# Kernel tuning notes

Hardware: AMD Instinct MI355X
Metric: run time of the kernel (lower is better)

Reference implementation:

```python
import jax, jax.numpy as jnp
import numpy as np

B, T, V, E, H, DE = 64, 52, 10000, 512, 512, 2048


def _lstm_cell(x, h, c, w_ih, w_hh, b_ih, b_hh):
    # torch.nn.LSTMCell gate order: i, f, g, o
    gates = x @ w_ih.T + h @ w_hh.T + b_ih + b_hh
    i, f, g, o = jnp.split(gates, 4, axis=-1)
    c2 = jax.nn.sigmoid(f) * c + jax.nn.sigmoid(i) * jnp.tanh(g)
    h2 = jax.nn.sigmoid(o) * jnp.tanh(c2)
    return h2, c2


def _run_dir(emb_seq, img, lens, p1, p2, fc_w, fc_b):
    # emb_seq: [B, Td, E]; img: [B, H]; lens: [B] sorted descending.
    # The torch loop slices h[:batch_size_t]; since lens is sorted descending,
    # that is equivalent to masking updates where t >= (len-1). Rows that fall
    # out of the active prefix are never read again, and their predictions stay 0.
    Bd, Td = emb_seq.shape[0], emb_seq.shape[1]
    Hd = img.shape[1]
    mask = jnp.arange(Td)[None, :] < (lens - 1)[:, None]  # [B, Td]
    z = jnp.zeros((Bd, Hd), emb_seq.dtype)

    def step(carry, xs):
        h, c, h1, c1 = carry
        x, m = xs
        m2 = m[:, None]
        hn, cn = _lstm_cell(x, h, c, *p1)
        h1n, c1n = _lstm_cell(jnp.concatenate([hn, img], axis=1), h1, c1, *p2)
        carry = (jnp.where(m2, hn, h), jnp.where(m2, cn, c),
                 jnp.where(m2, h1n, h1), jnp.where(m2, c1n, c1))
        preds = jnp.where(m2, h1n @ fc_w.T + fc_b, 0.0)  # [B, V]
        return carry, preds

    _, preds = jax.lax.scan(step, (z, z, z, z), (emb_seq.transpose(1, 0, 2), mask.T))
    return preds.transpose(1, 0, 2)  # [B, Td, V]


def setup_inputs():
    key = jax.random.key(0)
    ks = iter(jax.random.split(key, 48))

    def u(shape, a=-0.1, b=0.1):
        return jax.random.uniform(next(ks), shape, minval=a, maxval=b, dtype=jnp.float32)

    inp = {}
    inp['encoder_out'] = jax.random.normal(next(ks), (B, DE), dtype=jnp.float32)
    inp['encoded_captions'] = jax.random.randint(next(ks), (B, T), 0, V)
    cl = jax.random.randint(next(ks), (B, 1), 2, T + 1)
    inp['caption_lengths'] = cl.at[0, 0].set(T)  # ensure max decode length = T-1
    # embeddings (uniform -0.1..0.1 per init_weights)
    inp['emb_w'] = u((V, E))
    inp['emb_r_w'] = u((V, E))
    # LSTM cells: torch default init uniform(-1/sqrt(H), 1/sqrt(H))
    kH = 1.0 / np.sqrt(H)
    for name, din in [('1', E), ('2', 2 * H), ('r1', E), ('r2', 2 * H)]:
        inp['w_ih' + name] = u((4 * H, din), -kH, kH)
        inp['w_hh' + name] = u((4 * H, H), -kH, kH)
        inp['b_ih' + name] = u((4 * H,), -kH, kH)
        inp['b_hh' + name] = u((4 * H,), -kH, kH)
    kD = 1.0 / np.sqrt(DE)
    inp['img_f_w'] = u((H, DE), -kD, kD)
    inp['img_f_b'] = u((H,), -kD, kD)
    inp['img_b_w'] = u((H, DE), -kD, kD)
    inp['img_b_b'] = u((H,), -kD, kD)
    inp['fc_w'] = u((V, H))
    inp['fc_b'] = jnp.zeros((V,), jnp.float32)
    inp['fcr_w'] = u((V, H))
    inp['fcr_b'] = jnp.zeros((V,), jnp.float32)
    return inp


def reference(encoder_out, encoded_captions, caption_lengths, emb_w, emb_r_w,
              w_ih1, w_hh1, b_ih1, b_hh1, w_ih2, w_hh2, b_ih2, b_hh2,
              w_ihr1, w_hhr1, b_ihr1, b_hhr1, w_ihr2, w_hhr2, b_ihr2, b_hhr2,
              img_f_w, img_f_b, img_b_w, img_b_b, fc_w, fc_b, fcr_w, fcr_b):
    lens = caption_lengths[:, 0]
    order = jnp.argsort(-lens)  # descending, stable (jax argsort is stable)
    lens = lens[order]
    enc = encoder_out[order]
    caps = encoded_captions[order]
    Tc = caps.shape[1]
    # per-row reversal of the first len tokens; rest zero (matches torch loop)
    j = jnp.arange(Tc)[None, :]
    valid = j < lens[:, None]
    rev_idx = jnp.where(valid, lens[:, None] - 1 - j, 0)
    caps_rev = jnp.where(valid, jnp.take_along_axis(caps, rev_idx, axis=1), 0)
    emb = emb_w[caps]          # [B, T, E]
    emb_r = emb_r_w[caps_rev]  # [B, T, E]
    img_f = enc @ img_f_w.T + img_f_b
    img_r = enc @ img_b_w.T + img_b_b
    Td = Tc - 1  # max(decode_lengths); setup guarantees max(lens) == T
    preds = _run_dir(emb[:, :Td], img_f, lens,
                     (w_ih1, w_hh1, b_ih1, b_hh1), (w_ih2, w_hh2, b_ih2, b_hh2), fc_w, fc_b)
    preds_r = _run_dir(emb_r[:, :Td], img_r, lens,
                       (w_ihr1, w_hhr1, b_ihr1, b_hhr1), (w_ihr2, w_hhr2, b_ihr2, b_hhr2), fcr_w, fcr_b)
    return preds, preds_r, caps, caps_rev, lens - 1, order
```

## Files before the change

kernel.cpp:

```cpp
#include <hip/hip_runtime.h>
#include <stdint.h>

#define B64   64
#define T52   52
#define TD    51
#define V10K  10000
#define MP    3328
#define MR    3264
#define NPFC  10112

typedef float  f32x4  __attribute__((ext_vector_type(4)));
typedef __bf16 bf16x8 __attribute__((ext_vector_type(8)));
typedef unsigned int u32x4 __attribute__((ext_vector_type(4)));
typedef unsigned short ushort_t;

__device__ inline unsigned short f2bf(float f) {
  unsigned u = __builtin_bit_cast(unsigned, f);
  u += 0x7fffu + ((u >> 16) & 1u);
  return (unsigned short)(u >> 16);
}
__device__ inline unsigned pack2(float a, float b) {
  return (unsigned)f2bf(a) | ((unsigned)f2bf(b) << 16);
}
__device__ inline float sigm(float x) { return 1.f / (1.f + expf(-x)); }

__device__ inline void store2_sc(ushort_t* p, unsigned v) {
  asm volatile("global_store_short %0, %1, off sc1" :: "v"(p), "v"(v) : "memory");
}
__device__ inline void loadA16(const ushort_t* a, u32x4 (&h)[16]) {
  asm volatile(
    "global_load_dwordx4 %0,  %16, off sc1\n\t"
    "global_load_dwordx4 %1,  %16, off offset:64 sc1\n\t"
    "global_load_dwordx4 %2,  %16, off offset:128 sc1\n\t"
    "global_load_dwordx4 %3,  %16, off offset:192 sc1\n\t"
    "global_load_dwordx4 %4,  %16, off offset:256 sc1\n\t"
    "global_load_dwordx4 %5,  %16, off offset:320 sc1\n\t"
    "global_load_dwordx4 %6,  %16, off offset:384 sc1\n\t"
    "global_load_dwordx4 %7,  %16, off offset:448 sc1\n\t"
    "global_load_dwordx4 %8,  %16, off offset:512 sc1\n\t"
    "global_load_dwordx4 %9,  %16, off offset:576 sc1\n\t"
    "global_load_dwordx4 %10, %16, off offset:640 sc1\n\t"
    "global_load_dwordx4 %11, %16, off offset:704 sc1\n\t"
    "global_load_dwordx4 %12, %16, off offset:768 sc1\n\t"
    "global_load_dwordx4 %13, %16, off offset:832 sc1\n\t"
    "global_load_dwordx4 %14, %16, off offset:896 sc1\n\t"
    "global_load_dwordx4 %15, %16, off offset:960 sc1\n\t"
    "s_waitcnt vmcnt(0)"
    : "=&v"(h[0]),"=&v"(h[1]),"=&v"(h[2]),"=&v"(h[3]),
      "=&v"(h[4]),"=&v"(h[5]),"=&v"(h[6]),"=&v"(h[7]),
      "=&v"(h[8]),"=&v"(h[9]),"=&v"(h[10]),"=&v"(h[11]),
      "=&v"(h[12]),"=&v"(h[13]),"=&v"(h[14]),"=&v"(h[15])
    : "v"(a) : "memory");
}
__device__ inline void loadA32(const ushort_t* a, const ushort_t* b,
                               u32x4 (&ha)[16], u32x4 (&hb)[16]) {
  asm volatile(
    "global_load_dwordx4 %0,  %32, off sc1\n\t"
    "global_load_dwordx4 %1,  %32, off offset:64 sc1\n\t"
    "global_load_dwordx4 %2,  %32, off offset:128 sc1\n\t"
    "global_load_dwordx4 %3,  %32, off offset:192 sc1\n\t"
    "global_load_dwordx4 %4,  %32, off offset:256 sc1\n\t"
    "global_load_dwordx4 %5,  %32, off offset:320 sc1\n\t"
    "global_load_dwordx4 %6,  %32, off offset:384 sc1\n\t"
    "global_load_dwordx4 %7,  %32, off offset:448 sc1\n\t"
    "global_load_dwordx4 %8,  %32, off offset:512 sc1\n\t"
    "global_load_dwordx4 %9,  %32, off offset:576 sc1\n\t"
    "global_load_dwordx4 %10, %32, off offset:640 sc1\n\t"
    "global_load_dwordx4 %11, %32, off offset:704 sc1\n\t"
    "global_load_dwordx4 %12, %32, off offset:768 sc1\n\t"
    "global_load_dwordx4 %13, %32, off offset:832 sc1\n\t"
    "global_load_dwordx4 %14, %32, off offset:896 sc1\n\t"
    "global_load_dwordx4 %15, %32, off offset:960 sc1\n\t"
    "global_load_dwordx4 %16, %33, off sc1\n\t"
    "global_load_dwordx4 %17, %33, off offset:64 sc1\n\t"
    "global_load_dwordx4 %18, %33, off offset:128 sc1\n\t"
    "global_load_dwordx4 %19, %33, off offset:192 sc1\n\t"
    "global_load_dwordx4 %20, %33, off offset:256 sc1\n\t"
    "global_load_dwordx4 %21, %33, off offset:320 sc1\n\t"
    "global_load_dwordx4 %22, %33, off offset:384 sc1\n\t"
    "global_load_dwordx4 %23, %33, off offset:448 sc1\n\t"
    "global_load_dwordx4 %24, %33, off offset:512 sc1\n\t"
    "global_load_dwordx4 %25, %33, off offset:576 sc1\n\t"
    "global_load_dwordx4 %26, %33, off offset:640 sc1\n\t"
    "global_load_dwordx4 %27, %33, off offset:704 sc1\n\t"
    "global_load_dwordx4 %28, %33, off offset:768 sc1\n\t"
    "global_load_dwordx4 %29, %33, off offset:832 sc1\n\t"
    "global_load_dwordx4 %30, %33, off offset:896 sc1\n\t"
    "global_load_dwordx4 %31, %33, off offset:960 sc1\n\t"
    "s_waitcnt vmcnt(0)"
    : "=&v"(ha[0]),"=&v"(ha[1]),"=&v"(ha[2]),"=&v"(ha[3]),
      "=&v"(ha[4]),"=&v"(ha[5]),"=&v"(ha[6]),"=&v"(ha[7]),
      "=&v"(ha[8]),"=&v"(ha[9]),"=&v"(ha[10]),"=&v"(ha[11]),
      "=&v"(ha[12]),"=&v"(ha[13]),"=&v"(ha[14]),"=&v"(ha[15]),
      "=&v"(hb[0]),"=&v"(hb[1]),"=&v"(hb[2]),"=&v"(hb[3]),
      "=&v"(hb[4]),"=&v"(hb[5]),"=&v"(hb[6]),"=&v"(hb[7]),
      "=&v"(hb[8]),"=&v"(hb[9]),"=&v"(hb[10]),"=&v"(hb[11]),
      "=&v"(hb[12]),"=&v"(hb[13]),"=&v"(hb[14]),"=&v"(hb[15])
    : "v"(a), "v"(b) : "memory");
}

__global__ void k_prep(const int* __restrict__ cl, const int* __restrict__ caps,
                       float* __restrict__ out_caps, float* __restrict__ out_capr,
                       float* __restrict__ out_lm1, float* __restrict__ out_ord,
                       int* __restrict__ order_i, int* __restrict__ lensm1_i,
                       int* __restrict__ nvtab, int* __restrict__ capsS,
                       int* __restrict__ capsRev, int* __restrict__ cumtab,
                       int* __restrict__ rowmap)
{
  __shared__ int L[64], O[64], Ls_s[64], Cum[65];
  __shared__ int C_s[64][T52];
  int i = threadIdx.x;
  L[i] = cl[i];
  __syncthreads();
  if (i == 0) {
    for (int a = 0; a < 64; ++a) O[a] = a;
    for (int a = 1; a < 64; ++a) {
      int key = O[a], kl = L[key], b = a - 1;
      while (b >= 0 && L[O[b]] < kl) { O[b + 1] = O[b]; --b; }
      O[b + 1] = key;
    }
  }
  __syncthreads();
  int src = O[i];
  int Ls  = L[src];
  Ls_s[i] = Ls;
  order_i[i]  = src;
  lensm1_i[i] = Ls - 1;
  out_lm1[i]  = (float)(Ls - 1);
  out_ord[i]  = (float)src;
  for (int t = 0; t < T52; ++t) {
    int c = caps[src * T52 + t];
    C_s[i][t] = c;
    capsS[i * T52 + t]    = c;
    out_caps[i * T52 + t] = (float)c;
  }
  __syncthreads();
  for (int j = 0; j < T52; ++j) {
    int rv = (j < Ls) ? C_s[i][Ls - 1 - j] : 0;
    capsRev[i * T52 + j]  = rv;
    out_capr[i * T52 + j] = (float)rv;
  }
  if (i == 0) {
    int s = 0;
    for (int b = 0; b < 64; ++b) { Cum[b] = s; s += Ls_s[b] - 1; }
    Cum[64] = s;
  }
  __syncthreads();
  cumtab[i] = Cum[i];
  if (i == 0) cumtab[64] = Cum[64];
  for (int t = 0; t < Ls - 1; ++t) rowmap[Cum[i] + t] = i * TD + t;
  if (i < TD) {
    int nv = 0;
    for (int r = 0; r < 64; ++r) nv += (Ls_s[r] - 1 > i) ? 1 : 0;
    nvtab[i] = nv;
  }
}

__global__ void k_convert(const float* __restrict__ w_ih1, const float* __restrict__ w_ihr1,
                          const float* __restrict__ fc_w, const float* __restrict__ fcr_w,
                          const float* __restrict__ b_ih1, const float* __restrict__ b_hh1,
                          const float* __restrict__ b_ihr1, const float* __restrict__ b_hhr1,
                          const float* __restrict__ w_hh1, const float* __restrict__ w_hhr1,
                          const float* __restrict__ w_ih2, const float* __restrict__ w_ihr2,
                          const float* __restrict__ w_hh2, const float* __restrict__ w_hhr2,
                          const float* __restrict__ img_f_w, const float* __restrict__ img_b_w,
                          const float* __restrict__ b_ih2, const float* __restrict__ b_hh2,
                          const float* __restrict__ b_ihr2, const float* __restrict__ b_hhr2,
                          const float* __restrict__ enc, const int* __restrict__ order_i,
                          ushort_t* __restrict__ wih1bf, ushort_t* __restrict__ fcwbf,
                          ushort_t* __restrict__ whh1bf, ushort_t* __restrict__ wih2Lbf,
                          ushort_t* __restrict__ whh2bf, ushort_t* __restrict__ wih2Ibf,
                          ushort_t* __restrict__ imgwbf, ushort_t* __restrict__ encbf,
                          float* __restrict__ biasg1, float* __restrict__ biasg2)
{
  long long gid = (long long)blockIdx.x * blockDim.x + threadIdx.x;
  const long long C1 = 2048LL * 512 / 8;
  const long long CF = (long long)NPFC * 512 / 8;
  const long long bs  = 2 * C1 + 2 * CF;
  const long long bs2 = bs + 6 * C1;
  const long long bs3 = bs2 + 2 * C1;
  const long long bs4 = bs3 + 2 * C1;
  const long long bs5 = bs4 + 32768;
  if (gid < 2 * C1) {
    int dir = gid >= C1; long long cid = gid - (long long)dir * C1;
    const float* s = (dir ? w_ihr1 : w_ih1) + cid * 8;
    ushort_t* d = wih1bf + (long long)dir * 2048 * 512 + cid * 8;
    uint4 v;
    v.x = pack2(s[0], s[1]); v.y = pack2(s[2], s[3]);
    v.z = pack2(s[4], s[5]); v.w = pack2(s[6], s[7]);
    *(uint4*)d = v;
  } else if (gid < bs) {
    long long g2 = gid - 2 * C1; int dir = g2 >= CF;
    long long cid = g2 - (long long)dir * CF;
    long long row = cid >> 6; int k8 = (int)(cid & 63) * 8;
    ushort_t* d = fcwbf + (long long)dir * NPFC * 512 + row * 512 + k8;
    uint4 v;
    if (row < V10K) {
      const float* s = (dir ? fcr_w : fc_w) + row * 512 + k8;
      v.x = pack2(s[0], s[1]); v.y = pack2(s[2], s[3]);
      v.z = pack2(s[4], s[5]); v.w = pack2(s[6], s[7]);
    } else { v.x = v.y = v.z = v.w = 0u; }
    *(uint4*)d = v;
  } else if (gid < bs2) {
    long long e = gid - bs;
    int arr = (int)(e / (2 * C1));
    long long d2 = e - (long long)arr * 2 * C1;
    int dir = d2 >= C1;
    long long cid = d2 - (long long)dir * C1;
    long long row = cid >> 6; int k8 = (int)(cid & 63) * 8;
    const float* s;
    ushort_t* d;
    if (arr == 0)      { s = (dir ? w_hhr1 : w_hh1) + row * 512  + k8; d = whh1bf; }
    else if (arr == 1) { s = (dir ? w_ihr2 : w_ih2) + row * 1024 + k8; d = wih2Lbf; }
    else               { s = (dir ? w_hhr2 : w_hh2) + row * 512  + k8; d = whh2bf; }
    d += (long long)dir * 2048 * 512 + cid * 8;
    uint4 v;
    v.x = pack2(s[0], s[1]); v.y = pack2(s[2], s[3]);
    v.z = pack2(s[4], s[5]); v.w = pack2(s[6], s[7]);
    *(uint4*)d = v;
  } else if (gid < bs3) {
    long long e = gid - bs2; int dir = e >= C1;
    long long cid = e - (long long)dir * C1;
    long long row = cid >> 6; int k8 = (int)(cid & 63) * 8;
    const float* s = (dir ? w_ihr2 : w_ih2) + row * 1024 + 512 + k8;
    ushort_t* d = wih2Ibf + (long long)dir * 2048 * 512 + cid * 8;
    uint4 v;
    v.x = pack2(s[0], s[1]); v.y = pack2(s[2], s[3]);
    v.z = pack2(s[4], s[5]); v.w = pack2(s[6], s[7]);
    *(uint4*)d = v;
  } else if (gid < bs4) {
    long long e = gid - bs3; int dir = e >= C1;
    long long cid = e - (long long)dir * C1;
    long long row = cid >> 8; int c8 = (int)(cid & 255) * 8;
    const float* s = (dir ? img_b_w : img_f_w) + row * 2048 + c8;
    ushort_t* d = imgwbf + (long long)dir * 512 * 2048 + cid * 8;
    uint4 v;
    v.x = pack2(s[0], s[1]); v.y = pack2(s[2], s[3]);
    v.z = pack2(s[4], s[5]); v.w = pack2(s[6], s[7]);
    *(uint4*)d = v;
  } else if (gid < bs5) {
    long long cid = gid - bs4;
    int m = (int)(cid >> 8); int c8 = (int)(cid & 255) * 8;
    const float* s = enc + (long long)order_i[m & 63] * 2048 + c8;
    ushort_t* d = encbf + cid * 8;
    uint4 v;
    v.x = pack2(s[0], s[1]); v.y = pack2(s[2], s[3]);
    v.z = pack2(s[4], s[5]); v.w = pack2(s[6], s[7]);
    *(uint4*)d = v;
  } else {
    long long g3 = gid - bs5;
    if (g3 < 4096) {
      int dir = g3 >= 2048; int j = (int)(g3 & 2047);
      biasg1[dir * 2048 + j] = dir ? (b_ihr1[j] + b_hhr1[j]) : (b_ih1[j] + b_hh1[j]);
    } else if (g3 < 8192) {
      long long g4 = g3 - 4096;
      int dir = g4 >= 2048; int j = (int)(g4 & 2047);
      biasg2[dir * 2048 + j] = dir ? (b_ihr2[j] + b_hhr2[j]) : (b_ih2[j] + b_hh2[j]);
    }
  }
}

__global__ void k_gather(const float* __restrict__ emb_w, const float* __restrict__ emb_r_w,
                         const int* __restrict__ capsS, const int* __restrict__ capsRev,
                         const int* __restrict__ rowmap, const int* __restrict__ cumtab,
                         ushort_t* __restrict__ embA)
{
  long long gid = (long long)blockIdx.x * 256 + threadIdx.x;
  const long long CPD = (long long)MP * 512 / 8;
  if (gid >= 2 * CPD) return;
  int dir = gid >= CPD; long long cid = gid - (long long)dir * CPD;
  int c = (int)(cid >> 6); int k8 = (int)(cid & 63) * 8;
  ushort_t* d = embA + (long long)dir * MP * 512 + (long long)c * 512 + k8;
  uint4 v;
  if (c < cumtab[64]) {
    int m = rowmap[c];
    int b = m / TD, t = m - b * TD;
    int row = dir ? capsRev[b * T52 + t] : capsS[b * T52 + t];
    const float* s = (dir ? emb_r_w : emb_w) + (long long)row * 512 + k8;
    v.x = pack2(s[0], s[1]); v.y = pack2(s[2], s[3]);
    v.z = pack2(s[4], s[5]); v.w = pack2(s[6], s[7]);
  } else { v.x = v.y = v.z = v.w = 0u; }
  *(uint4*)d = v;
}

template<int MODE>
__global__ __launch_bounds__(256)
void k_gemm(const ushort_t* __restrict__ A0, long long As,
            const ushort_t* __restrict__ B0, long long Bs,
            const float* __restrict__ bias0, const float* __restrict__ bias1,
            void* __restrict__ out0, long long Os,
            int Nreal, int K, const int* __restrict__ mlim)
{
  long long tm = (long long)blockIdx.x * 128;
  if (mlim && tm >= mlim[64]) return;
  __shared__ ushort_t Ab[128 * 32];
  __shared__ ushort_t Bb[128 * 32];
  int dirz = blockIdx.z;
  const ushort_t* A = A0 + dirz * As;
  const ushort_t* Bm = B0 + dirz * Bs;
  const float* bias = dirz ? bias1 : bias0;
  int tid = threadIdx.x;
  int lane = tid & 63, wid = tid >> 6;
  int wr = wid >> 1, wc = wid & 1;
  long long tn = (long long)blockIdx.y * 128;
  f32x4 acc[4][4] = {};
  int c0 = tid, c1 = tid + 256;
  const ushort_t* Ag0 = A + (tm + (c0 >> 2)) * K + (c0 & 3) * 8;
  const ushort_t* Ag1 = A + (tm + (c1 >> 2)) * K + (c1 & 3) * 8;
  const ushort_t* Bg0 = Bm + (tn + (c0 >> 2)) * K + (c0 & 3) * 8;
  const ushort_t* Bg1 = Bm + (tn + (c1 >> 2)) * K + (c1 & 3) * 8;
  int KK = K >> 5;
  for (int kk = 0; kk < KK; ++kk) {
    uint4 va0 = *(const uint4*)(Ag0 + kk * 32);
    uint4 va1 = *(const uint4*)(Ag1 + kk * 32);
    uint4 vb0 = *(const uint4*)(Bg0 + kk * 32);
    uint4 vb1 = *(const uint4*)(Bg1 + kk * 32);
    __syncthreads();
    *(uint4*)&Ab[c0 * 8] = va0;
    *(uint4*)&Ab[c1 * 8] = va1;
    *(uint4*)&Bb[c0 * 8] = vb0;
    *(uint4*)&Bb[c1 * 8] = vb1;
    __syncthreads();
    int koff = (lane >> 4) * 8;
    bf16x8 av[4], bv[4];
    #pragma unroll
    for (int mi = 0; mi < 4; ++mi)
      av[mi] = *(const bf16x8*)&Ab[(wr * 64 + mi * 16 + (lane & 15)) * 32 + koff];
    #pragma unroll
    for (int ni = 0; ni < 4; ++ni)
      bv[ni] = *(const bf16x8*)&Bb[(wc * 64 + ni * 16 + (lane & 15)) * 32 + koff];
    #pragma unroll
    for (int mi = 0; mi < 4; ++mi)
      #pragma unroll
      for (int ni = 0; ni < 4; ++ni)
        acc[mi][ni] = __builtin_amdgcn_mfma_f32_16x16x32_bf16(av[mi], bv[ni], acc[mi][ni], 0, 0, 0);
  }
  #pragma unroll
  for (int mi = 0; mi < 4; ++mi) {
    #pragma unroll
    for (int rr = 0; rr < 4; ++rr) {
      long long m = tm + wr * 64 + mi * 16 + ((lane >> 4) * 4) + rr;
      if (MODE == 0) {
        float* orow = (float*)out0 + dirz * Os + m * (long long)Nreal;
        #pragma unroll
        for (int ni = 0; ni < 4; ++ni) {
          int n = (int)tn + wc * 64 + ni * 16 + (lane & 15);
          orow[n] = acc[mi][ni][rr] + bias[n];
        }
      } else if (MODE == 2) {
        float bm = bias[m];
        float* orow = (float*)out0 + dirz * Os + m * (long long)Nreal;
        #pragma unroll
        for (int ni = 0; ni < 4; ++ni) {
          int n = (int)tn + wc * 64 + ni * 16 + (lane & 15);
          if (n < Nreal) orow[n] = acc[mi][ni][rr] + bm;
        }
      } else {
        ushort_t* orow = (ushort_t*)out0 + dirz * Os + m * (long long)Nreal;
        #pragma unroll
        for (int ni = 0; ni < 4; ++ni) {
          int n = (int)tn + wc * 64 + ni * 16 + (lane & 15);
          orow[n] = f2bf(acc[mi][ni][rr] + bias[n]);
        }
      }
    }
  }
}

__global__ __launch_bounds__(256)
void k_fc(const ushort_t* __restrict__ A0, const ushort_t* __restrict__ B0,
          const float* __restrict__ bias0, const float* __restrict__ bias1,
          float* __restrict__ out0, const int* __restrict__ rowmap,
          const int* __restrict__ cumtab)
{
  const long long PRED = (long long)MR * V10K;
  int Mc = cumtab[64];
  long long tm = (long long)blockIdx.x * 128;
  if (tm >= Mc) return;
  __shared__ ushort_t Ab[128 * 32];
  __shared__ ushort_t Bb[128 * 32];
  int dirz = blockIdx.z;
  const ushort_t* A = A0 + (long long)dirz * MP * 512;
  const ushort_t* Bm = B0 + (long long)dirz * NPFC * 512;
  const float* bias = dirz ? bias1 : bias0;
  float* out = out0 + (long long)dirz * PRED;
  int tid = threadIdx.x;
  int lane = tid & 63, wid = tid >> 6;
  int wr = wid >> 1, wc = wid & 1;
  long long tn = (long long)blockIdx.y * 128;
  f32x4 acc[4][4] = {};
  int c0 = tid, c1 = tid + 256;
  const ushort_t* Ag0 = A + (tm + (c0 >> 2)) * 512 + (c0 & 3) * 8;
  const ushort_t* Ag1 = A + (tm + (c1 >> 2)) * 512 + (c1 & 3) * 8;
  const ushort_t* Bg0 = Bm + (tn + (c0 >> 2)) * 512 + (c0 & 3) * 8;
  const ushort_t* Bg1 = Bm + (tn + (c1 >> 2)) * 512 + (c1 & 3) * 8;
  for (int kk = 0; kk < 16; ++kk) {
    uint4 va0 = *(const uint4*)(Ag0 + kk * 32);
    uint4 va1 = *(const uint4*)(Ag1 + kk * 32);
    uint4 vb0 = *(const uint4*)(Bg0 + kk * 32);
    uint4 vb1 = *(const uint4*)(Bg1 + kk * 32);
    __syncthreads();
    *(uint4*)&Ab[c0 * 8] = va0;
    *(uint4*)&Ab[c1 * 8] = va1;
    *(uint4*)&Bb[c0 * 8] = vb0;
    *(uint4*)&Bb[c1 * 8] = vb1;
    __syncthreads();
    int koff = (lane >> 4) * 8;
    bf16x8 av[4], bv[4];
    #pragma unroll
    for (int mi = 0; mi < 4; ++mi)
      av[mi] = *(const bf16x8*)&Ab[(wr * 64 + mi * 16 + (lane & 15)) * 32 + koff];
    #pragma unroll
    for (int ni = 0; ni < 4; ++ni)
      bv[ni] = *(const bf16x8*)&Bb[(wc * 64 + ni * 16 + (lane & 15)) * 32 + koff];
    #pragma unroll
    for (int mi = 0; mi < 4; ++mi)
      #pragma unroll
      for (int ni = 0; ni < 4; ++ni)
        acc[mi][ni] = __builtin_amdgcn_mfma_f32_16x16x32_bf16(av[mi], bv[ni], acc[mi][ni], 0, 0, 0);
  }
  #pragma unroll
  for (int mi = 0; mi < 4; ++mi) {
    #pragma unroll
    for (int rr = 0; rr < 4; ++rr) {
      long long c = tm + wr * 64 + mi * 16 + ((lane >> 4) * 4) + rr;
      if (c < Mc) {
        int m = rowmap[c];
        float* orow = out + (long long)m * V10K;
        #pragma unroll
        for (int ni = 0; ni < 4; ++ni) {
          int n = (int)tn + wc * 64 + ni * 16 + (lane & 15);
          if (n < V10K) orow[n] = acc[mi][ni][rr] + bias[n];
        }
      }
    }
  }
}

__global__ __launch_bounds__(256)
void k_zero(float* __restrict__ outF, const int* __restrict__ lensm1_i)
{
  const long long PRED = (long long)MR * V10K;
  int m = blockIdx.x;
  int b = m / TD, t = m - b * TD;
  if (t < lensm1_i[b]) return;
  float4 z = {0.f, 0.f, 0.f, 0.f};
  float* r0 = outF + (long long)m * V10K;
  float* r1 = outF + PRED + (long long)m * V10K;
  for (int i = threadIdx.x; i < 2500; i += 256) {
    ((float4*)r0)[i] = z;
    ((float4*)r1)[i] = z;
  }
}

__global__ __launch_bounds__(128, 1)
void k_rec(const ushort_t* __restrict__ whh1bf, const ushort_t* __restrict__ wih2Lbf,
           const ushort_t* __restrict__ whh2bf, const float* __restrict__ xg1,
           const float* __restrict__ xg2imgT,
           ushort_t* __restrict__ h1hist,
           ushort_t* __restrict__ h2buf,
           ushort_t* __restrict__ h2allbf,
           const int* __restrict__ nvtab, const int* __restrict__ cumtab,
           int* __restrict__ slots)
{
  const int bid = blockIdx.x;
  const bool isL2 = bid >= 128;
  const int idx = isL2 ? bid - 128 : bid;
  const int dir = idx >> 6, sub = idx & 63, half = sub >> 5, ht = sub & 31;
  const int tid = threadIdx.x;
  const int lane = tid & 63, mt = tid >> 6;
  const int l15 = lane & 15, l4 = lane >> 4;
  const int jl = ht * 16 + l15;
  const int rbase = half * 32 + mt * 16;
  const int r0 = rbase + l4 * 4;

  __shared__ ushort_t Wl[32768];
  __shared__ ushort_t Wi[32768];
  __shared__ int nv_s[64];
  __shared__ int cum_s[64];

  {
    const ushort_t* src = (isL2 ? whh2bf : whh1bf) + (long long)dir * 2048 * 512;
    #pragma unroll
    for (int i = 0; i < 32; ++i) {
      int c = tid + i * 128;
      int nl = c >> 6;
      int kb = (c & 63) * 16;
      int row = (nl >> 4) * 512 + ht * 16 + (nl & 15);
      u32x4 v = *(const u32x4*)(src + (long long)row * 512 + (long long)(c & 63) * 8);
      *(u32x4*)((char*)Wl + nl * 1024 + (kb ^ ((nl & 7) << 4))) = v;
    }
    if (isL2) {
      const ushort_t* src2 = wih2Lbf + (long long)dir * 2048 * 512;
      #pragma unroll
      for (int i = 0; i < 32; ++i) {
        int c = tid + i * 128;
        int nl = c >> 6;
        int kb = (c & 63) * 16;
        int row = (nl >> 4) * 512 + ht * 16 + (nl & 15);
        u32x4 v = *(const u32x4*)(src2 + (long long)row * 512 + (long long)(c & 63) * 8);
        *(u32x4*)((char*)Wi + nl * 1024 + (kb ^ ((nl & 7) << 4))) = v;
      }
    }
    if (tid < TD) nv_s[tid] = nvtab[tid];
    if (tid < 64) cum_s[tid] = cumtab[tid];
  }
  __syncthreads();

  int* aS = slots + (dir * 2 + half) * 32;
  int* bS = slots + 128 + (dir * 2 + half) * 32;

  if (!isL2) {
    f32x4 creg = {0.f, 0.f, 0.f, 0.f};
    for (int t = 0; t < TD; ++t) {
      bool act = (rbase < nv_s[t]);
      float xs[4][4];
      if (act) {
        const float* xb = xg1 + (long long)dir * MP * 2048;
        #pragma unroll
        for (int rr = 0; rr < 4; ++rr) {
          const float* xr = xb + (long long)(cum_s[r0 + rr] + t) * 2048;
          #pragma unroll
          for (int g = 0; g < 4; ++g)
            xs[g][rr] = xr[g * 512 + jl];
        }
      }
      if (t > 0) {
        if (mt == 0) {
          for (;;) {
            int v = __hip_atomic_load(&aS[lane & 31], __ATOMIC_RELAXED, __HIP_MEMORY_SCOPE_AGENT);
            if (__all(v >= t)) break;
          }
        }
        __syncthreads();
      }
      if (act) {
        const ushort_t* hsrc = h1hist + ((long long)t * 2 + dir) * (64 * 512);
        u32x4 hv[16];
        loadA16(hsrc + (long long)(rbase + l15) * 512 + l4 * 8, hv);
        f32x4 acc[4] = {};
        #pragma unroll
        for (int kk = 0; kk < 16; ++kk) {
          bf16x8 av = __builtin_bit_cast(bf16x8, hv[kk]);
          int kb = kk * 64 + l4 * 16;
          #pragma unroll
          for (int g = 0; g < 4; ++g) {
            bf16x8 bv = *(const bf16x8*)((const char*)Wl + (g * 16 + l15) * 1024 + (kb ^ ((l15 & 7) << 4)));
            acc[g] = __builtin_amdgcn_mfma_f32_16x16x32_bf16(av, bv, acc[g], 0, 0, 0);
          }
        }
        ushort_t* hdst = h1hist + ((long long)(t + 1) * 2 + dir) * (64 * 512);
        f32x4 cn;
        #pragma unroll
        for (int rr = 0; rr < 4; ++rr) {
          float gi = acc[0][rr] + xs[0][rr];
          float gf = acc[1][rr] + xs[1][rr];
          float gg = acc[2][rr] + xs[2][rr];
          float go = acc[3][rr] + xs[3][rr];
          float c = sigm(gf) * creg[rr] + sigm(gi) * tanhf(gg);
          float h = sigm(go) * tanhf(c);
          cn[rr] = c;
          store2_sc(hdst + (long long)(r0 + rr) * 512 + jl, (unsigned)f2bf(h));
        }
        creg = cn;
      }
      __syncthreads();
      if (tid == 0)
        __hip_atomic_store(&aS[ht], t + 1, __ATOMIC_RELAXED, __HIP_MEMORY_SCOPE_AGENT);
    }
  } else {
    f32x4 xv2[4];
    {
      const float* xg = xg2imgT + (long long)dir * (2048 * 64);
      #pragma unroll
      for (int g = 0; g < 4; ++g)
        xv2[g] = *(const f32x4*)(xg + (long long)(g * 512 + jl) * 64 + r0);
    }
    f32x4 creg = {0.f, 0.f, 0.f, 0.f};
    for (int t = 0; t < TD; ++t) {
      if (mt == 0) {
        for (;;) {
          int va = __hip_atomic_load(&aS[lane & 31], __ATOMIC_RELAXED, __HIP_MEMORY_SCOPE_AGENT);
          int vb = __hip_atomic_load(&bS[lane & 31], __ATOMIC_RELAXED, __HIP_MEMORY_SCOPE_AGENT);
          if (__all((va >= t + 1) & (vb >= t))) break;
        }
      }
      __syncthreads();
      int nv = nv_s[t];
      if (rbase < nv) {
        const ushort_t* h1s = h1hist + ((long long)(t + 1) * 2 + dir) * (64 * 512);
        const ushort_t* h2s = h2buf + ((long long)((t + 1) & 1) * 2 + dir) * (64 * 512);
        u32x4 ha[16], hb[16];
        loadA32(h1s + (long long)(rbase + l15) * 512 + l4 * 8,
                h2s + (long long)(rbase + l15) * 512 + l4 * 8, ha, hb);
        f32x4 acc[4] = {};
        #pragma unroll
        for (int kk = 0; kk < 16; ++kk) {
          bf16x8 av = __builtin_bit_cast(bf16x8, ha[kk]);
          int kb = kk * 64 + l4 * 16;
          #pragma unroll
          for (int g = 0; g < 4; ++g) {
            bf16x8 bv = *(const bf16x8*)((const char*)Wi + (g * 16 + l15) * 1024 + (kb ^ ((l15 & 7) << 4)));
            acc[g] = __builtin_amdgcn_mfma_f32_16x16x32_bf16(av, bv, acc[g], 0, 0, 0);
          }
        }
        #pragma unroll
        for (int kk = 0; kk < 16; ++kk) {
          bf16x8 av = __builtin_bit_cast(bf16x8, hb[kk]);
          int kb = kk * 64 + l4 * 16;
          #pragma unroll
          for (int g = 0; g < 4; ++g) {
            bf16x8 bv = *(const bf16x8*)((const char*)Wl + (g * 16 + l15) * 1024 + (kb ^ ((l15 & 7) << 4)));
            acc[g] = __builtin_amdgcn_mfma_f32_16x16x32_bf16(av, bv, acc[g], 0, 0, 0);
          }
        }
        ushort_t* h2n = h2buf + ((long long)(t & 1) * 2 + dir) * (64 * 512);
        ushort_t* h2a = h2allbf + (long long)dir * MP * 512;
        f32x4 cn;
        #pragma unroll
        for (int rr = 0; rr < 4; ++rr) {
          float gi = acc[0][rr] + xv2[0][rr];
          float gf = acc[1][rr] + xv2[1][rr];
          float gg = acc[2][rr] + xv2[2][rr];
          float go = acc[3][rr] + xv2[3][rr];
          float c = sigm(gf) * creg[rr] + sigm(gi) * tanhf(gg);
          float h = sigm(go) * tanhf(c);
          cn[rr] = c;
          ushort_t hbb = f2bf(h);
          store2_sc(h2n + (long long)(r0 + rr) * 512 + jl, (unsigned)hbb);
          if (r0 + rr < nv)
            h2a[((long long)(cum_s[r0 + rr] + t)) * 512 + jl] = hbb;
        }
        creg = cn;
      }
      __syncthreads();
      if (tid == 0)
        __hip_atomic_store(&bS[ht], t + 1, __ATOMIC_RELAXED, __HIP_MEMORY_SCOPE_AGENT);
    }
  }
}

extern "C" void kernel_launch(void* const* d_in, const int* in_sizes, int n_in,
                              void* d_out, int out_size, void* d_ws, size_t ws_size,
                              hipStream_t stream)
{
  const float* enc     = (const float*)d_in[0];
  const int*   caps    = (const int*)d_in[1];
  const int*   cl      = (const int*)d_in[2];
  const float* emb_w   = (const float*)d_in[3];
  const float* emb_r_w = (const float*)d_in[4];
  const float* w_ih1   = (const float*)d_in[5];
  const float* w_hh1   = (const float*)d_in[6];
  const float* b_ih1   = (const float*)d_in[7];
  const float* b_hh1   = (const float*)d_in[8];
  const float* w_ih2   = (const float*)d_in[9];
  const float* w_hh2   = (const float*)d_in[10];
  const float* b_ih2   = (const float*)d_in[11];
  const float* b_hh2   = (const float*)d_in[12];
  const float* w_ihr1  = (const float*)d_in[13];
  const float* w_hhr1  = (const float*)d_in[14];
  const float* b_ihr1  = (const float*)d_in[15];
  const float* b_hhr1  = (const float*)d_in[16];
  const float* w_ihr2  = (const float*)d_in[17];
  const float* w_hhr2  = (const float*)d_in[18];
  const float* b_ihr2  = (const float*)d_in[19];
  const float* b_hhr2  = (const float*)d_in[20];
  const float* img_f_w = (const float*)d_in[21];
  const float* img_f_b = (const float*)d_in[22];
  const float* img_b_w = (const float*)d_in[23];
  const float* img_b_b = (const float*)d_in[24];
  const float* fc_w    = (const float*)d_in[25];
  const float* fc_b    = (const float*)d_in[26];
  const float* fcr_w   = (const float*)d_in[27];
  const float* fcr_b   = (const float*)d_in[28];

  float* outF = (float*)d_out;
  const long long PRED = (long long)MR * V10K;
  float* o_caps = outF + 2 * PRED;
  float* o_capr = o_caps + B64 * T52;
  float* o_lm1  = o_capr + B64 * T52;
  float* o_ord  = o_lm1 + B64;
  float*    xg1       = outF;
  ushort_t* whh1bf    = (ushort_t*)(outF + 27500000);
  ushort_t* wih2Lbf   = (ushort_t*)(outF + 28600000);
  ushort_t* whh2bf    = (ushort_t*)(outF + 29700000);
  ushort_t* h1hist    = (ushort_t*)(outF + 31000000);
  ushort_t* wih2Ibf   = (ushort_t*)(outF + 34600000);
  ushort_t* imgwbf    = (ushort_t*)(outF + 35700000);
  ushort_t* encbf     = (ushort_t*)(outF + 36800000);
  ushort_t* imgbf     = (ushort_t*)(outF + 37000000);

  char* w = (char*)d_ws;
  auto alloc = [&](size_t bytes) -> char* {
    char* p = w; w += (bytes + 255) & ~(size_t)255; return p;
  };
  int*      order_i  = (int*)alloc(64 * 4);
  int*      lensm1_i = (int*)alloc(64 * 4);
  int*      nvtab    = (int*)alloc(64 * 4);
  int*      cumtab   = (int*)alloc(65 * 4);
  int*      rowmap   = (int*)alloc(MR * 4);
  int*      capsS    = (int*)alloc(B64 * T52 * 4);
  int*      capsRev  = (int*)alloc(B64 * T52 * 4);
  float*    biasg1   = (float*)alloc(2 * 2048 * 4);
  float*    biasg2   = (float*)alloc(2 * 2048 * 4);
  float*    xg2imgT  = (float*)alloc((size_t)2 * 2048 * 64 * 4);
  char*     stateBase = alloc(262144 + 1024);
  ushort_t* h2buf = (ushort_t*)stateBase;
  int*      slotp = (int*)(stateBase + 262144);
  ushort_t* embA    = (ushort_t*)alloc((size_t)2 * MP * 512 * 2);
  ushort_t* wih1bf  = (ushort_t*)alloc((size_t)2 * 2048 * 512 * 2);
  ushort_t* fcwbf   = (ushort_t*)alloc((size_t)2 * NPFC * 512 * 2);
  ushort_t* h2allbf = (ushort_t*)alloc((size_t)2 * MP * 512 * 2);

  hipMemsetAsync(stateBase, 0, 262144 + 1024, stream);
  hipMemsetAsync(h1hist, 0, 131072, stream);

  k_prep<<<1, 64, 0, stream>>>(cl, caps, o_caps, o_capr, o_lm1, o_ord,
                               order_i, lensm1_i, nvtab, capsS, capsRev,
                               cumtab, rowmap);
  k_convert<<<11360, 256, 0, stream>>>(w_ih1, w_ihr1, fc_w, fcr_w,
                                       b_ih1, b_hh1, b_ihr1, b_hhr1,
                                       w_hh1, w_hhr1, w_ih2, w_ihr2, w_hh2, w_hhr2,
                                       img_f_w, img_b_w, b_ih2, b_hh2, b_ihr2, b_hhr2,
                                       enc, order_i,
                                       wih1bf, fcwbf, whh1bf, wih2Lbf, whh2bf,
                                       wih2Ibf, imgwbf, encbf, biasg1, biasg2);
  k_gather<<<1664, 256, 0, stream>>>(emb_w, emb_r_w, capsS, capsRev,
                                     rowmap, cumtab, embA);
  k_gemm<3><<<dim3(1, 4, 2), 256, 0, stream>>>(encbf, 0LL,
                                               imgwbf, 512LL * 2048,
                                               img_f_b, img_b_b,
                                               imgbf, 128LL * 512,
                                               512, 2048, nullptr);
  k_gemm<2><<<dim3(16, 1, 2), 256, 0, stream>>>(wih2Ibf, 2048LL * 512,
                                                imgbf, 128LL * 512,
                                                biasg2, biasg2 + 2048,
                                                xg2imgT, 2048LL * 64,
                                                64, 512, nullptr);
  k_gemm<0><<<dim3(26, 16, 2), 256, 0, stream>>>(embA, (long long)MP * 512,
                                                 wih1bf, 2048LL * 512,
                                                 biasg1, biasg1 + 2048,
                                                 xg1, (long long)MP * 2048,
                                                 2048, 512, cumtab);
  k_rec<<<256, 128, 0, stream>>>(whh1bf, wih2Lbf, whh2bf, xg1, xg2imgT,
                                 h1hist, h2buf, h2allbf, nvtab, cumtab, slotp);
  k_zero<<<MR, 256, 0, stream>>>(outF, lensm1_i);
  k_fc<<<dim3(26, 79, 2), 256, 0, stream>>>(h2allbf, fcwbf, fc_b, fcr_b,
                                            outF, rowmap, cumtab);
}
```

Measured before the change: 694.0 us.

## Replace block barriers with per-wave flags and split layer-2 waits

```diff
diff --git a/kernel.cpp b/kernel.cpp
--- a/kernel.cpp
+++ b/kernel.cpp
@@ -51,52 +51,6 @@
       "=&v"(h[8]),"=&v"(h[9]),"=&v"(h[10]),"=&v"(h[11]),
       "=&v"(h[12]),"=&v"(h[13]),"=&v"(h[14]),"=&v"(h[15])
     : "v"(a) : "memory");
-}
-__device__ inline void loadA32(const ushort_t* a, const ushort_t* b,
-                               u32x4 (&ha)[16], u32x4 (&hb)[16]) {
-  asm volatile(
-    "global_load_dwordx4 %0,  %32, off sc1\n\t"
-    "global_load_dwordx4 %1,  %32, off offset:64 sc1\n\t"
-    "global_load_dwordx4 %2,  %32, off offset:128 sc1\n\t"
-    "global_load_dwordx4 %3,  %32, off offset:192 sc1\n\t"
-    "global_load_dwordx4 %4,  %32, off offset:256 sc1\n\t"
-    "global_load_dwordx4 %5,  %32, off offset:320 sc1\n\t"
-    "global_load_dwordx4 %6,  %32, off offset:384 sc1\n\t"
-    "global_load_dwordx4 %7,  %32, off offset:448 sc1\n\t"
-    "global_load_dwordx4 %8,  %32, off offset:512 sc1\n\t"
-    "global_load_dwordx4 %9,  %32, off offset:576 sc1\n\t"
-    "global_load_dwordx4 %10, %32, off offset:640 sc1\n\t"
-    "global_load_dwordx4 %11, %32, off offset:704 sc1\n\t"
-    "global_load_dwordx4 %12, %32, off offset:768 sc1\n\t"
-    "global_load_dwordx4 %13, %32, off offset:832 sc1\n\t"
-    "global_load_dwordx4 %14, %32, off offset:896 sc1\n\t"
-    "global_load_dwordx4 %15, %32, off offset:960 sc1\n\t"
-    "global_load_dwordx4 %16, %33, off sc1\n\t"
-    "global_load_dwordx4 %17, %33, off offset:64 sc1\n\t"
-    "global_load_dwordx4 %18, %33, off offset:128 sc1\n\t"
-    "global_load_dwordx4 %19, %33, off offset:192 sc1\n\t"
-    "global_load_dwordx4 %20, %33, off offset:256 sc1\n\t"
-    "global_load_dwordx4 %21, %33, off offset:320 sc1\n\t"
-    "global_load_dwordx4 %22, %33, off offset:384 sc1\n\t"
-    "global_load_dwordx4 %23, %33, off offset:448 sc1\n\t"
-    "global_load_dwordx4 %24, %33, off offset:512 sc1\n\t"
-    "global_load_dwordx4 %25, %33, off offset:576 sc1\n\t"
-    "global_load_dwordx4 %26, %33, off offset:640 sc1\n\t"
-    "global_load_dwordx4 %27, %33, off offset:704 sc1\n\t"
-    "global_load_dwordx4 %28, %33, off offset:768 sc1\n\t"
-    "global_load_dwordx4 %29, %33, off offset:832 sc1\n\t"
-    "global_load_dwordx4 %30, %33, off offset:896 sc1\n\t"
-    "global_load_dwordx4 %31, %33, off offset:960 sc1\n\t"
-    "s_waitcnt vmcnt(0)"
-    : "=&v"(ha[0]),"=&v"(ha[1]),"=&v"(ha[2]),"=&v"(ha[3]),
-      "=&v"(ha[4]),"=&v"(ha[5]),"=&v"(ha[6]),"=&v"(ha[7]),
-      "=&v"(ha[8]),"=&v"(ha[9]),"=&v"(ha[10]),"=&v"(ha[11]),
-      "=&v"(ha[12]),"=&v"(ha[13]),"=&v"(ha[14]),"=&v"(ha[15]),
-      "=&v"(hb[0]),"=&v"(hb[1]),"=&v"(hb[2]),"=&v"(hb[3]),
-      "=&v"(hb[4]),"=&v"(hb[5]),"=&v"(hb[6]),"=&v"(hb[7]),
-      "=&v"(hb[8]),"=&v"(hb[9]),"=&v"(hb[10]),"=&v"(hb[11]),
-      "=&v"(hb[12]),"=&v"(hb[13]),"=&v"(hb[14]),"=&v"(hb[15])
-    : "v"(a), "v"(b) : "memory");
 }
 
 __global__ void k_prep(const int* __restrict__ cl, const int* __restrict__ caps,
@@ -507,8 +461,10 @@
   }
   __syncthreads();
 
-  int* aS = slots + (dir * 2 + half) * 32;
-  int* bS = slots + 128 + (dir * 2 + half) * 32;
+  int* aG = slots + (dir * 2 + half) * 64;
+  int* bG = slots + 256 + (dir * 2 + half) * 64;
+  const int myFlag = (ht << 1) | mt;
+  const int pollIdx = ((lane & 31) << 1) | mt;
 
   if (!isL2) {
     f32x4 creg = {0.f, 0.f, 0.f, 0.f};
@@ -526,13 +482,10 @@
         }
       }
       if (t > 0) {
-        if (mt == 0) {
-          for (;;) {
-            int v = __hip_atomic_load(&aS[lane & 31], __ATOMIC_RELAXED, __HIP_MEMORY_SCOPE_AGENT);
-            if (__all(v >= t)) break;
-          }
-        }
-        __syncthreads();
+        for (;;) {
+          int v = __hip_atomic_load(&aG[pollIdx], __ATOMIC_RELAXED, __HIP_MEMORY_SCOPE_AGENT);
+          if (__all(v >= t)) break;
+        }
       }
       if (act) {
         const ushort_t* hsrc = h1hist + ((long long)t * 2 + dir) * (64 * 512);
@@ -564,9 +517,9 @@
         }
         creg = cn;
       }
-      __syncthreads();
-      if (tid == 0)
-        __hip_atomic_store(&aS[ht], t + 1, __ATOMIC_RELAXED, __HIP_MEMORY_SCOPE_AGENT);
+      asm volatile("s_waitcnt vmcnt(0)" ::: "memory");
+      if (lane == 0)
+        __hip_atomic_store(&aG[myFlag], t + 1, __ATOMIC_RELAXED, __HIP_MEMORY_SCOPE_AGENT);
     }
   } else {
     f32x4 xv2[4];
@@ -578,22 +531,17 @@
     }
     f32x4 creg = {0.f, 0.f, 0.f, 0.f};
     for (int t = 0; t < TD; ++t) {
-      if (mt == 0) {
-        for (;;) {
-          int va = __hip_atomic_load(&aS[lane & 31], __ATOMIC_RELAXED, __HIP_MEMORY_SCOPE_AGENT);
-          int vb = __hip_atomic_load(&bS[lane & 31], __ATOMIC_RELAXED, __HIP_MEMORY_SCOPE_AGENT);
-          if (__all((va >= t + 1) & (vb >= t))) break;
-        }
-      }
-      __syncthreads();
+      bool act = (rbase < nv_s[t]);
       int nv = nv_s[t];
-      if (rbase < nv) {
+      f32x4 acc[4] = {};
+      for (;;) {
+        int v = __hip_atomic_load(&aG[pollIdx], __ATOMIC_RELAXED, __HIP_MEMORY_SCOPE_AGENT);
+        if (__all(v >= t + 1)) break;
+      }
+      if (act) {
         const ushort_t* h1s = h1hist + ((long long)(t + 1) * 2 + dir) * (64 * 512);
-        const ushort_t* h2s = h2buf + ((long long)((t + 1) & 1) * 2 + dir) * (64 * 512);
-        u32x4 ha[16], hb[16];
-        loadA32(h1s + (long long)(rbase + l15) * 512 + l4 * 8,
-                h2s + (long long)(rbase + l15) * 512 + l4 * 8, ha, hb);
-        f32x4 acc[4] = {};
+        u32x4 ha[16];
+        loadA16(h1s + (long long)(rbase + l15) * 512 + l4 * 8, ha);
         #pragma unroll
         for (int kk = 0; kk < 16; ++kk) {
           bf16x8 av = __builtin_bit_cast(bf16x8, ha[kk]);
@@ -604,6 +552,15 @@
             acc[g] = __builtin_amdgcn_mfma_f32_16x16x32_bf16(av, bv, acc[g], 0, 0, 0);
           }
         }
+      }
+      for (;;) {
+        int v = __hip_atomic_load(&bG[pollIdx], __ATOMIC_RELAXED, __HIP_MEMORY_SCOPE_AGENT);
+        if (__all(v >= t)) break;
+      }
+      if (act) {
+        const ushort_t* h2s = h2buf + ((long long)((t + 1) & 1) * 2 + dir) * (64 * 512);
+        u32x4 hb[16];
+        loadA16(h2s + (long long)(rbase + l15) * 512 + l4 * 8, hb);
         #pragma unroll
         for (int kk = 0; kk < 16; ++kk) {
           bf16x8 av = __builtin_bit_cast(bf16x8, hb[kk]);
@@ -633,9 +590,9 @@
         }
         creg = cn;
       }
-      __syncthreads();
-      if (tid == 0)
-        __hip_atomic_store(&bS[ht], t + 1, __ATOMIC_RELAXED, __HIP_MEMORY_SCOPE_AGENT);
+      asm volatile("s_waitcnt vmcnt(0)" ::: "memory");
+      if (lane == 0)
+        __hip_atomic_store(&bG[myFlag], t + 1, __ATOMIC_RELAXED, __HIP_MEMORY_SCOPE_AGENT);
     }
   }
 }
@@ -704,7 +661,7 @@
   float*    biasg1   = (float*)alloc(2 * 2048 * 4);
   float*    biasg2   = (float*)alloc(2 * 2048 * 4);
   float*    xg2imgT  = (float*)alloc((size_t)2 * 2048 * 64 * 4);
-  char*     stateBase = alloc(262144 + 1024);
+  char*     stateBase = alloc(262144 + 4096);
   ushort_t* h2buf = (ushort_t*)stateBase;
   int*      slotp = (int*)(stateBase + 262144);
   ushort_t* embA    = (ushort_t*)alloc((size_t)2 * MP * 512 * 2);
@@ -712,7 +669,7 @@
   ushort_t* fcwbf   = (ushort_t*)alloc((size_t)2 * NPFC * 512 * 2);
   ushort_t* h2allbf = (ushort_t*)alloc((size_t)2 * MP * 512 * 2);
 
-  hipMemsetAsync(stateBase, 0, 262144 + 1024, stream);
+  hipMemsetAsync(stateBase, 0, 262144 + 4096, stream);
   hipMemsetAsync(h1hist, 0, 131072, stream);
 
   k_prep<<<1, 64, 0, stream>>>(cl, caps, o_caps, o_capr, o_lm1, o_ord,
```

New measurement: 724.3 us. +4.4%, slower.

## Fuse embedding gather into convert kernel and widen GEMM K-tile with swizzled LDS

Applied to the files above, without the earlier changes.

```diff
diff --git a/kernel.cpp b/kernel.cpp
--- a/kernel.cpp
+++ b/kernel.cpp
@@ -167,20 +167,26 @@
                           const float* __restrict__ b_ih2, const float* __restrict__ b_hh2,
                           const float* __restrict__ b_ihr2, const float* __restrict__ b_hhr2,
                           const float* __restrict__ enc, const int* __restrict__ order_i,
+                          const float* __restrict__ emb_w, const float* __restrict__ emb_r_w,
+                          const int* __restrict__ capsS, const int* __restrict__ capsRev,
+                          const int* __restrict__ rowmap, const int* __restrict__ cumtab,
                           ushort_t* __restrict__ wih1bf, ushort_t* __restrict__ fcwbf,
                           ushort_t* __restrict__ whh1bf, ushort_t* __restrict__ wih2Lbf,
                           ushort_t* __restrict__ whh2bf, ushort_t* __restrict__ wih2Ibf,
                           ushort_t* __restrict__ imgwbf, ushort_t* __restrict__ encbf,
+                          ushort_t* __restrict__ embA,
                           float* __restrict__ biasg1, float* __restrict__ biasg2)
 {
   long long gid = (long long)blockIdx.x * blockDim.x + threadIdx.x;
   const long long C1 = 2048LL * 512 / 8;
   const long long CF = (long long)NPFC * 512 / 8;
+  const long long CPD = (long long)MP * 512 / 8;
   const long long bs  = 2 * C1 + 2 * CF;
   const long long bs2 = bs + 6 * C1;
   const long long bs3 = bs2 + 2 * C1;
   const long long bs4 = bs3 + 2 * C1;
   const long long bs5 = bs4 + 32768;
+  const long long bs6 = bs5 + 2 * CPD;
   if (gid < 2 * C1) {
     int dir = gid >= C1; long long cid = gid - (long long)dir * C1;
     const float* s = (dir ? w_ihr1 : w_ih1) + cid * 8;
@@ -247,8 +253,23 @@
     v.x = pack2(s[0], s[1]); v.y = pack2(s[2], s[3]);
     v.z = pack2(s[4], s[5]); v.w = pack2(s[6], s[7]);
     *(uint4*)d = v;
+  } else if (gid < bs6) {
+    long long e = gid - bs5;
+    int dir = e >= CPD; long long cid = e - (long long)dir * CPD;
+    int c = (int)(cid >> 6); int k8 = (int)(cid & 63) * 8;
+    ushort_t* d = embA + (long long)dir * MP * 512 + (long long)c * 512 + k8;
+    uint4 v;
+    if (c < cumtab[64]) {
+      int m = rowmap[c];
+      int b = m / TD, t = m - b * TD;
+      int row = dir ? capsRev[b * T52 + t] : capsS[b * T52 + t];
+      const float* s = (dir ? emb_r_w : emb_w) + (long long)row * 512 + k8;
+      v.x = pack2(s[0], s[1]); v.y = pack2(s[2], s[3]);
+      v.z = pack2(s[4], s[5]); v.w = pack2(s[6], s[7]);
+    } else { v.x = v.y = v.z = v.w = 0u; }
+    *(uint4*)d = v;
   } else {
-    long long g3 = gid - bs5;
+    long long g3 = gid - bs6;
     if (g3 < 4096) {
       int dir = g3 >= 2048; int j = (int)(g3 & 2047);
       biasg1[dir * 2048 + j] = dir ? (b_ihr1[j] + b_hhr1[j]) : (b_ih1[j] + b_hh1[j]);
@@ -258,29 +279,6 @@
       biasg2[dir * 2048 + j] = dir ? (b_ihr2[j] + b_hhr2[j]) : (b_ih2[j] + b_hh2[j]);
     }
   }
-}
-
-__global__ void k_gather(const float* __restrict__ emb_w, const float* __restrict__ emb_r_w,
-                         const int* __restrict__ capsS, const int* __restrict__ capsRev,
-                         const int* __restrict__ rowmap, const int* __restrict__ cumtab,
-                         ushort_t* __restrict__ embA)
-{
-  long long gid = (long long)blockIdx.x * 256 + threadIdx.x;
-  const long long CPD = (long long)MP * 512 / 8;
-  if (gid >= 2 * CPD) return;
-  int dir = gid >= CPD; long long cid = gid - (long long)dir * CPD;
-  int c = (int)(cid >> 6); int k8 = (int)(cid & 63) * 8;
-  ushort_t* d = embA + (long long)dir * MP * 512 + (long long)c * 512 + k8;
-  uint4 v;
-  if (c < cumtab[64]) {
-    int m = rowmap[c];
-    int b = m / TD, t = m - b * TD;
-    int row = dir ? capsRev[b * T52 + t] : capsS[b * T52 + t];
-    const float* s = (dir ? emb_r_w : emb_w) + (long long)row * 512 + k8;
-    v.x = pack2(s[0], s[1]); v.y = pack2(s[2], s[3]);
-    v.z = pack2(s[4], s[5]); v.w = pack2(s[6], s[7]);
-  } else { v.x = v.y = v.z = v.w = 0u; }
-  *(uint4*)d = v;
 }
 
 template<int MODE>
@@ -293,8 +291,8 @@
 {
   long long tm = (long long)blockIdx.x * 128;
   if (mlim && tm >= mlim[64]) return;
-  __shared__ ushort_t Ab[128 * 32];
-  __shared__ ushort_t Bb[128 * 32];
+  __shared__ ushort_t Ab[128 * 64];
+  __shared__ ushort_t Bb[128 * 64];
   int dirz = blockIdx.z;
   const ushort_t* A = A0 + dirz * As;
   const ushort_t* Bm = B0 + dirz * Bs;
@@ -304,36 +302,47 @@
   int wr = wid >> 1, wc = wid & 1;
   long long tn = (long long)blockIdx.y * 128;
   f32x4 acc[4][4] = {};
-  int c0 = tid, c1 = tid + 256;
-  const ushort_t* Ag0 = A + (tm + (c0 >> 2)) * K + (c0 & 3) * 8;
-  const ushort_t* Ag1 = A + (tm + (c1 >> 2)) * K + (c1 & 3) * 8;
-  const ushort_t* Bg0 = Bm + (tn + (c0 >> 2)) * K + (c0 & 3) * 8;
-  const ushort_t* Bg1 = Bm + (tn + (c1 >> 2)) * K + (c1 & 3) * 8;
-  int KK = K >> 5;
+  int KK = K >> 6;
   for (int kk = 0; kk < KK; ++kk) {
-    uint4 va0 = *(const uint4*)(Ag0 + kk * 32);
-    uint4 va1 = *(const uint4*)(Ag1 + kk * 32);
-    uint4 vb0 = *(const uint4*)(Bg0 + kk * 32);
-    uint4 vb1 = *(const uint4*)(Bg1 + kk * 32);
+    uint4 va[4], vb[4];
+    #pragma unroll
+    for (int p = 0; p < 4; ++p) {
+      int g = tid + p * 256;
+      int row = g >> 3, gc = g & 7;
+      va[p] = *(const uint4*)(A + (tm + row) * K + kk * 64 + gc * 8);
+      vb[p] = *(const uint4*)(Bm + (tn + row) * K + kk * 64 + gc * 8);
+    }
     __syncthreads();
-    *(uint4*)&Ab[c0 * 8] = va0;
-    *(uint4*)&Ab[c1 * 8] = va1;
-    *(uint4*)&Bb[c0 * 8] = vb0;
-    *(uint4*)&Bb[c1 * 8] = vb1;
+    #pragma unroll
+    for (int p = 0; p < 4; ++p) {
+      int g = tid + p * 256;
+      int row = g >> 3, gc = g & 7;
+      int slot = gc ^ (row & 7);
+      *(uint4*)&Ab[row * 64 + slot * 8] = va[p];
+      *(uint4*)&Bb[row * 64 + slot * 8] = vb[p];
+    }
     __syncthreads();
-    int koff = (lane >> 4) * 8;
-    bf16x8 av[4], bv[4];
-    #pragma unroll
-    for (int mi = 0; mi < 4; ++mi)
-      av[mi] = *(const bf16x8*)&Ab[(wr * 64 + mi * 16 + (lane & 15)) * 32 + koff];
-    #pragma unroll
-    for (int ni = 0; ni < 4; ++ni)
-      bv[ni] = *(const bf16x8*)&Bb[(wc * 64 + ni * 16 + (lane & 15)) * 32 + koff];
-    #pragma unroll
-    for (int mi = 0; mi < 4; ++mi)
+    #pragma unroll
+    for (int sub = 0; sub < 2; ++sub) {
+      bf16x8 av[4], bv[4];
       #pragma unroll
-      for (int ni = 0; ni < 4; ++ni)
-        acc[mi][ni] = __builtin_amdgcn_mfma_f32_16x16x32_bf16(av[mi], bv[ni], acc[mi][ni], 0, 0, 0);
+      for (int mi = 0; mi < 4; ++mi) {
+        int row = wr * 64 + mi * 16 + (lane & 15);
+        int gcol = sub * 4 + (lane >> 4);
+        av[mi] = *(const bf16x8*)&Ab[row * 64 + (gcol ^ (row & 7)) * 8];
+      }
+      #pragma unroll
+      for (int ni = 0; ni < 4; ++ni) {
+        int row = wc * 64 + ni * 16 + (lane & 15);
+        int gcol = sub * 4 + (lane >> 4);
+        bv[ni] = *(const bf16x8*)&Bb[row * 64 + (gcol ^ (row & 7)) * 8];
+      }
+      #pragma unroll
+      for (int mi = 0; mi < 4; ++mi)
+        #pragma unroll
+        for (int ni = 0; ni < 4; ++ni)
+          acc[mi][ni] = __builtin_amdgcn_mfma_f32_16x16x32_bf16(av[mi], bv[ni], acc[mi][ni], 0, 0, 0);
+    }
   }
   #pragma unroll
   for (int mi = 0; mi < 4; ++mi) {
@@ -377,8 +386,8 @@
   int Mc = cumtab[64];
   long long tm = (long long)blockIdx.x * 128;
   if (tm >= Mc) return;
-  __shared__ ushort_t Ab[128 * 32];
-  __shared__ ushort_t Bb[128 * 32];
+  __shared__ ushort_t Ab[128 * 64];
+  __shared__ ushort_t Bb[128 * 64];
   int dirz = blockIdx.z;
   const ushort_t* A = A0 + (long long)dirz * MP * 512;
   const ushort_t* Bm = B0 + (long long)dirz * NPFC * 512;
@@ -389,35 +398,46 @@
   int wr = wid >> 1, wc = wid & 1;
   long long tn = (long long)blockIdx.y * 128;
   f32x4 acc[4][4] = {};
-  int c0 = tid, c1 = tid + 256;
-  const ushort_t* Ag0 = A + (tm + (c0 >> 2)) * 512 + (c0 & 3) * 8;
-  const ushort_t* Ag1 = A + (tm + (c1 >> 2)) * 512 + (c1 & 3) * 8;
-  const ushort_t* Bg0 = Bm + (tn + (c0 >> 2)) * 512 + (c0 & 3) * 8;
-  const ushort_t* Bg1 = Bm + (tn + (c1 >> 2)) * 512 + (c1 & 3) * 8;
-  for (int kk = 0; kk < 16; ++kk) {
-    uint4 va0 = *(const uint4*)(Ag0 + kk * 32);
-    uint4 va1 = *(const uint4*)(Ag1 + kk * 32);
-    uint4 vb0 = *(const uint4*)(Bg0 + kk * 32);
-    uint4 vb1 = *(const uint4*)(Bg1 + kk * 32);
+  for (int kk = 0; kk < 8; ++kk) {
+    uint4 va[4], vb[4];
+    #pragma unroll
+    for (int p = 0; p < 4; ++p) {
+      int g = tid + p * 256;
+      int row = g >> 3, gc = g & 7;
+      va[p] = *(const uint4*)(A + (tm + row) * 512 + kk * 64 + gc * 8);
+      vb[p] = *(const uint4*)(Bm + (tn + row) * 512 + kk * 64 + gc * 8);
+    }
     __syncthreads();
-    *(uint4*)&Ab[c0 * 8] = va0;
-    *(uint4*)&Ab[c1 * 8] = va1;
-    *(uint4*)&Bb[c0 * 8] = vb0;
-    *(uint4*)&Bb[c1 * 8] = vb1;
+    #pragma unroll
+    for (int p = 0; p < 4; ++p) {
+      int g = tid + p * 256;
+      int row = g >> 3, gc = g & 7;
+      int slot = gc ^ (row & 7);
+      *(uint4*)&Ab[row * 64 + slot * 8] = va[p];
+      *(uint4*)&Bb[row * 64 + slot * 8] = vb[p];
+    }
     __syncthreads();
-    int koff = (lane >> 4) * 8;
-    bf16x8 av[4], bv[4];
-    #pragma unroll
-    for (int mi = 0; mi < 4; ++mi)
-      av[mi] = *(const bf16x8*)&Ab[(wr * 64 + mi * 16 + (lane & 15)) * 32 + koff];
-    #pragma unroll
-    for (int ni = 0; ni < 4; ++ni)
-      bv[ni] = *(const bf16x8*)&Bb[(wc * 64 + ni * 16 + (lane & 15)) * 32 + koff];
-    #pragma unroll
-    for (int mi = 0; mi < 4; ++mi)
+    #pragma unroll
+    for (int sub = 0; sub < 2; ++sub) {
+      bf16x8 av[4], bv[4];
       #pragma unroll
-      for (int ni = 0; ni < 4; ++ni)
-        acc[mi][ni] = __builtin_amdgcn_mfma_f32_16x16x32_bf16(av[mi], bv[ni], acc[mi][ni], 0, 0, 0);
+      for (int mi = 0; mi < 4; ++mi) {
+        int row = wr * 64 + mi * 16 + (lane & 15);
+        int gcol = sub * 4 + (lane >> 4);
+        av[mi] = *(const bf16x8*)&Ab[row * 64 + (gcol ^ (row & 7)) * 8];
+      }
+      #pragma unroll
+      for (int ni = 0; ni < 4; ++ni) {
+        int row = wc * 64 + ni * 16 + (lane & 15);
+        int gcol = sub * 4 + (lane >> 4);
+        bv[ni] = *(const bf16x8*)&Bb[row * 64 + (gcol ^ (row & 7)) * 8];
+      }
+      #pragma unroll
+      for (int mi = 0; mi < 4; ++mi)
+        #pragma unroll
+        for (int ni = 0; ni < 4; ++ni)
+          acc[mi][ni] = __builtin_amdgcn_mfma_f32_16x16x32_bf16(av[mi], bv[ni], acc[mi][ni], 0, 0, 0);
+    }
   }
   #pragma unroll
   for (int mi = 0; mi < 4; ++mi) {
@@ -718,15 +738,14 @@
   k_prep<<<1, 64, 0, stream>>>(cl, caps, o_caps, o_capr, o_lm1, o_ord,
                                order_i, lensm1_i, nvtab, capsS, capsRev,
                                cumtab, rowmap);
-  k_convert<<<11360, 256, 0, stream>>>(w_ih1, w_ihr1, fc_w, fcr_w,
+  k_convert<<<13024, 256, 0, stream>>>(w_ih1, w_ihr1, fc_w, fcr_w,
                                        b_ih1, b_hh1, b_ihr1, b_hhr1,
                                        w_hh1, w_hhr1, w_ih2, w_ihr2, w_hh2, w_hhr2,
                                        img_f_w, img_b_w, b_ih2, b_hh2, b_ihr2, b_hhr2,
-                                       enc, order_i,
+                                       enc, order_i, emb_w, emb_r_w,
+                                       capsS, capsRev, rowmap, cumtab,
                                        wih1bf, fcwbf, whh1bf, wih2Lbf, whh2bf,
-                                       wih2Ibf, imgwbf, encbf, biasg1, biasg2);
-  k_gather<<<1664, 256, 0, stream>>>(emb_w, emb_r_w, capsS, capsRev,
-                                     rowmap, cumtab, embA);
+                                       wih2Ibf, imgwbf, encbf, embA, biasg1, biasg2);
   k_gemm<3><<<dim3(1, 4, 2), 256, 0, stream>>>(encbf, 0LL,
                                                imgwbf, 512LL * 2048,
                                                img_f_b, img_b_b,
```

After: 929.2 us. 1.34x slower.
